# Kernel tuning notes

Measured on AMD Instinct MI355X. Metric: run time of the kernel, lower is better.

## Reference

```python
import jax, jax.numpy as jnp
import numpy as np

N = 50000      # num nodes
E = 500000     # num edges
D = 128        # in_dim == out_dim
H = 8          # num heads
DPH = D // H   # 16, out_dim_per_head
DFF = 2 * D    # FFN hidden
EPS_BN = 1e-5


def setup_inputs() -> dict:
    key = jax.random.key(0)
    ks = jax.random.split(key, 16)
    s = 0.05
    inp = {
        "x": jax.random.normal(ks[0], (N, D), dtype=jnp.float32),
        "edge_index": jax.random.randint(ks[1], (2, E), 0, N, dtype=jnp.int64),
        # attention projections (no bias, use_bias=False); stored as [in, out]
        "WQ": jax.random.normal(ks[2], (D, D), dtype=jnp.float32) * s,
        "WK": jax.random.normal(ks[3], (D, D), dtype=jnp.float32) * s,
        "WV": jax.random.normal(ks[4], (D, D), dtype=jnp.float32) * s,
        # output projection O (has bias by default)
        "WO": jax.random.normal(ks[5], (D, D), dtype=jnp.float32) * s,
        "bO": jnp.zeros((D,), dtype=jnp.float32),
        # FFN
        "W1": jax.random.normal(ks[6], (D, DFF), dtype=jnp.float32) * s,
        "b1": jnp.zeros((DFF,), dtype=jnp.float32),
        "W2": jax.random.normal(ks[7], (DFF, D), dtype=jnp.float32) * s,
        "b2": jnp.zeros((D,), dtype=jnp.float32),
        # batch norms (affine)
        "g1": jnp.ones((D,), dtype=jnp.float32),
        "be1": jnp.zeros((D,), dtype=jnp.float32),
        "g2": jnp.ones((D,), dtype=jnp.float32),
        "be2": jnp.zeros((D,), dtype=jnp.float32),
    }
    return inp


def _batch_norm(h, g, b):
    # training-mode BatchNorm1d over node (batch) dim, biased variance
    mu = jnp.mean(h, axis=0)
    var = jnp.var(h, axis=0)
    return g * (h - mu) * jax.lax.rsqrt(var + EPS_BN) + b


def _forward(x, edge_index, WQ, WK, WV, WO, bO, W1, b1, W2, b2, g1, be1, g2, be2):
    src = edge_index[0]  # j (source / neighbor)
    dst = edge_index[1]  # i (target, softmax segment index)

    Q = (x @ WQ).reshape(N, H, DPH)
    K = (x @ WK).reshape(N, H, DPH)
    V = (x @ WV).reshape(N, H, DPH)

    # edge-wise scores: [E, H]
    score = jnp.sum(Q[dst] * K[src], axis=-1) / jnp.sqrt(jnp.float32(DPH))
    score = jnp.clip(score, -5.0, 5.0)

    # segment softmax over edges grouped by destination node (per head)
    seg_max = jax.ops.segment_max(score, dst, num_segments=N)      # [N, H]
    seg_max = jnp.where(jnp.isfinite(seg_max), seg_max, 0.0)       # empty segs
    ex = jnp.exp(score - seg_max[dst])                             # [E, H]
    seg_sum = jax.ops.segment_sum(ex, dst, num_segments=N)         # [N, H]
    alpha = ex / (seg_sum[dst] + 1e-16)                            # [E, H]

    # weighted message + scatter-add aggregation
    msg = V[src] * alpha[..., None]                                # [E, H, DPH]
    agg = jax.ops.segment_sum(msg, dst, num_segments=N)            # [N, H, DPH]
    h = agg.reshape(N, D)

    # output projection + residual (in_dim == out_dim, no proj) + BN
    h = h @ WO + bO
    h = x + h
    h = _batch_norm(h, g1, be1)

    # FFN + residual + BN
    h2 = h
    h = jax.nn.relu(h @ W1 + b1)
    h = h @ W2 + b2
    h = h2 + h
    h = _batch_norm(h, g2, be2)
    return h


def reference(x, edge_index, WQ, WK, WV, WO, bO, W1, b1, W2, b2, g1, be1, g2, be2):
    return _forward(x, edge_index, WQ, WK, WV, WO, bO, W1, b1, W2, b2, g1, be1, g2, be2)
```

## Files before the change

### kernel.cpp

```cpp
#include <hip/hip_runtime.h>

#define DEV __device__ __forceinline__

constexpr int N = 50000;
constexpr int E = 500000;
constexpr int D = 128;
constexpr int DFF = 256;
constexpr int NBANK = 64;

typedef __attribute__((ext_vector_type(8))) short bfrag8;
typedef __attribute__((ext_vector_type(4))) float f32x4;

DEV unsigned short f2b(float f) {
    unsigned u = __float_as_uint(f);
    unsigned r = (u + 0x7FFFu + ((u >> 16) & 1u)) >> 16;
    return (unsigned short)r;
}
DEV unsigned pack2(float a, float b) {
    return (unsigned)f2b(a) | ((unsigned)f2b(b) << 16);
}
DEV float b2f(unsigned short v) { return __uint_as_float(((unsigned)v) << 16); }
DEV float lo16(unsigned u) { return __uint_as_float(u << 16); }
DEV float hi16(unsigned u) { return __uint_as_float(u & 0xFFFF0000u); }

constexpr float QSCALE = 0.36067376022224085f;
constexpr float CLIP2 = 7.2134752044448170f;

constexpr size_t AL(size_t x) { return (x + 511) & ~(size_t)511; }
constexpr size_t OFF_COUNTS = 0;
constexpr size_t OFF_CURSORS = AL(OFF_COUNTS + (size_t)N * 4);
constexpr size_t OFF_BANK1 = AL(OFF_CURSORS + (size_t)N * 4);
constexpr size_t OFF_BANK2 = AL(OFF_BANK1 + NBANK * 256 * 4);
constexpr size_t OFF_DONE = OFF_BANK2 + NBANK * 256 * 4;
constexpr size_t ZERO_END = OFF_DONE + 512;
constexpr size_t ZW = ZERO_END / 4;
constexpr size_t OFF_OFFS = AL(ZERO_END);
constexpr size_t OFF_BSUM = AL(OFF_OFFS + (size_t)N * 4);
constexpr size_t OFF_BPREF = AL(OFF_BSUM + 1024);
constexpr size_t OFF_SS1 = AL(OFF_BPREF + 1024);
constexpr size_t OFF_SS2 = AL(OFF_SS1 + 1024);
constexpr size_t OFF_B1P = AL(OFF_SS2 + 1024);
constexpr size_t OFF_CSR = AL(OFF_B1P + 1024);
constexpr size_t OFF_WQKVP = AL(OFF_CSR + (size_t)E * 4);
constexpr size_t OFF_WOP = AL(OFF_WQKVP + 49152 * 2);
constexpr size_t OFF_W1PF = AL(OFF_WOP + 16384 * 2);
constexpr size_t OFF_W1P = AL(OFF_W1PF + 32768 * 4);
constexpr size_t OFF_W2P = AL(OFF_W1P + 32768 * 2);
constexpr size_t OFF_Q = AL(OFF_W2P + 32768 * 2);
constexpr size_t OFF_KV = AL(OFF_Q + (size_t)N * 128 * 2);
constexpr size_t OFF_AGG = AL(OFF_KV + (size_t)N * 256 * 2);
constexpr size_t OFF_Y = AL(OFF_AGG + (size_t)N * 128 * 2);
constexpr size_t OFF_T = AL(OFF_Y + (size_t)N * 128 * 2);
constexpr size_t OFF_XB = AL(OFF_T + (size_t)N * 128 * 2);

__global__ void prep_w(const float* __restrict__ WQ, const float* __restrict__ WK,
                       const float* __restrict__ WV, const float* __restrict__ WO,
                       const float* __restrict__ W1, const float* __restrict__ W2,
                       unsigned short* __restrict__ WQKVp, unsigned short* __restrict__ WOp,
                       float* __restrict__ W1pf, unsigned short* __restrict__ W2p,
                       unsigned* __restrict__ zbase) {
    if (blockIdx.x >= 512) {
        size_t i = (size_t)(blockIdx.x - 512) * 256 + threadIdx.x;
        if (i < ZW) zbase[i] = 0u;
        return;
    }
    int gid = blockIdx.x * 256 + threadIdx.x;
    if (gid < 49152) {
        int s = gid >> 14, r = gid & 16383;
        int nt = r >> 11, kb = (r >> 9) & 3, lane = (r >> 3) & 63, j = r & 7;
        int n = nt * 16 + (lane & 15);
        int k = kb * 32 + (lane >> 4) * 8 + j;
        const float* W = (s == 0) ? WQ : (s == 1) ? WK : WV;
        WQKVp[gid] = f2b(W[k * 128 + n]);
    } else if (gid < 65536) {
        int r = gid - 49152;
        int nt = r >> 11, kb = (r >> 9) & 3, lane = (r >> 3) & 63, j = r & 7;
        int n = nt * 16 + (lane & 15);
        int k = kb * 32 + (lane >> 4) * 8 + j;
        WOp[r] = f2b(WO[k * 128 + n]);
    } else if (gid < 98304) {
        int r = gid - 65536;
        int nt = r >> 11, kb = (r >> 9) & 3, lane = (r >> 3) & 63, j = r & 7;
        int n = nt * 16 + (lane & 15);
        int k = kb * 32 + (lane >> 4) * 8 + j;
        W1pf[r] = W1[k * 256 + n];
    } else {
        int r = gid - 98304;
        int nt = r >> 12, kb = (r >> 9) & 7, lane = (r >> 3) & 63, j = r & 7;
        int n = nt * 16 + (lane & 15);
        int k = kb * 32 + (lane >> 4) * 8 + j;
        W2p[r] = f2b(W2[k * 128 + n]);
    }
}

__global__ void scan_a(const int* __restrict__ counts, int* __restrict__ offs,
                       int* __restrict__ bsum, int* __restrict__ bpref,
                       int* __restrict__ done) {
    __shared__ int sm[256];
    __shared__ int ticket;
    int t = threadIdx.x;
    int gi = blockIdx.x * 256 + t;
    int v = (gi < N) ? counts[gi] : 0;
    sm[t] = v;
    __syncthreads();
    for (int o = 1; o < 256; o <<= 1) {
        int x = (t >= o) ? sm[t - o] : 0;
        __syncthreads();
        sm[t] += x;
        __syncthreads();
    }
    if (gi < N) offs[gi] = sm[t] - v;
    if (t == 255) bsum[blockIdx.x] = sm[255];
    __threadfence();
    if (t == 0) ticket = atomicAdd(done, 1);
    __syncthreads();
    if (ticket == (int)gridDim.x - 1) {
        int bv = (t < (int)gridDim.x) ? atomicAdd(&bsum[t], 0) : 0;
        sm[t] = bv;
        __syncthreads();
        for (int o = 1; o < 256; o <<= 1) {
            int x = (t >= o) ? sm[t - o] : 0;
            __syncthreads();
            sm[t] += x;
            __syncthreads();
        }
        bpref[t] = sm[t] - bv;
    }
}

__global__ void fill_k(const int* __restrict__ eidx, const int* __restrict__ offs,
                       const int* __restrict__ bpref,
                       int* __restrict__ cursors, int* __restrict__ csr) {
    int e = blockIdx.x * 256 + threadIdx.x;
    if (e < E) {
        int d = eidx[E + e];
        int p = atomicAdd(&cursors[d], 1);
        csr[offs[d] + bpref[d >> 8] + p] = eidx[e];
    }
}

__global__ __launch_bounds__(256) void qkv_k(const float* __restrict__ x,
                                             const unsigned short* __restrict__ WQKVp,
                                             unsigned short* __restrict__ q,
                                             unsigned short* __restrict__ kv,
                                             unsigned short* __restrict__ xb,
                                             const int* __restrict__ eidx,
                                             int* __restrict__ counts, int nqkv) {
    if ((int)blockIdx.x >= nqkv) {
        int e = ((int)blockIdx.x - nqkv) * 256 + threadIdx.x;
        if (e < E) atomicAdd(&counts[eidx[E + e]], 1);
        return;
    }
    __shared__ unsigned short As[64][136];
    __shared__ unsigned short Cs[64][136];
    const int tid = threadIdx.x;
    const int lane = tid & 63, wave = tid >> 6;
    const int quad = lane >> 4, l15 = lane & 15;
    const int wr = wave >> 1, wc = wave & 1;
    const int row0 = blockIdx.x * 64;

#pragma unroll
    for (int it = 0; it < 4; it++) {
        int c = tid + it * 256;
        int r = c >> 4, k8 = (c & 15) * 8;
        int grow = row0 + r;
        uint4 val = {0u, 0u, 0u, 0u};
        if (grow < N) {
            const float* ap = x + (size_t)grow * 128 + k8;
            float4 f0 = *(const float4*)ap;
            float4 f1 = *(const float4*)(ap + 4);
            val.x = pack2(f0.x, f0.y);
            val.y = pack2(f0.z, f0.w);
            val.z = pack2(f1.x, f1.y);
            val.w = pack2(f1.z, f1.w);
        }
        *(uint4*)&As[r][k8] = val;
    }
    __syncthreads();

#pragma unroll
    for (int j = 0; j < 4; j++) {
        int idx = tid + j * 256;
        int u = idx >> 4, col8 = (idx & 15) * 8;
        int grow = row0 + u;
        if (grow < N) *(uint4*)(xb + (size_t)grow * 128 + col8) = *(const uint4*)&As[u][col8];
    }

    for (int s = 0; s < 3; s++) {
        f32x4 acc[2][4];
#pragma unroll
        for (int i = 0; i < 2; i++)
#pragma unroll
            for (int j = 0; j < 4; j++) acc[i][j] = (f32x4){0.f, 0.f, 0.f, 0.f};
#pragma unroll
        for (int ks = 0; ks < 4; ks++) {
            int k0 = ks * 32 + quad * 8;
            bfrag8 a0 = *(const bfrag8*)&As[wr * 32 + l15][k0];
            bfrag8 a1 = *(const bfrag8*)&As[wr * 32 + 16 + l15][k0];
#pragma unroll
            for (int jn = 0; jn < 4; jn++) {
                int nt = wc * 4 + jn;
                bfrag8 b = *(const bfrag8*)(WQKVp + ((((size_t)s * 8 + nt) * 4 + ks) * 64 + lane) * 8);
                acc[0][jn] = __builtin_amdgcn_mfma_f32_16x16x32_bf16(a0, b, acc[0][jn], 0, 0, 0);
                acc[1][jn] = __builtin_amdgcn_mfma_f32_16x16x32_bf16(a1, b, acc[1][jn], 0, 0, 0);
            }
        }
        if (s) __syncthreads();
        float sc = (s == 0) ? QSCALE : 1.0f;
#pragma unroll
        for (int i = 0; i < 2; i++) {
            int rb = wr * 32 + i * 16 + quad * 4;
#pragma unroll
            for (int jn = 0; jn < 4; jn++) {
                int cl = wc * 64 + jn * 16 + l15;
#pragma unroll
                for (int r = 0; r < 4; r++) Cs[rb + r][cl] = f2b(acc[i][jn][r] * sc);
            }
        }
        __syncthreads();
#pragma unroll
        for (int j = 0; j < 4; j++) {
            int idx = tid + j * 256;
            int u = idx >> 4, col8 = (idx & 15) * 8;
            int grow = row0 + u;
            if (grow < N) {
                uint4 v = *(const uint4*)&Cs[u][col8];
                if (s == 0)
                    *(uint4*)(q + (size_t)grow * 128 + col8) = v;
                else
                    *(uint4*)(kv + (size_t)grow * 256 + (s == 2 ? 128 : 0) + col8) = v;
            }
        }
    }
}

__global__ __launch_bounds__(256) void attn_k(const unsigned short* __restrict__ qb,
                                              const unsigned short* __restrict__ kv,
                                              const int* __restrict__ csr,
                                              const int* __restrict__ offs,
                                              const int* __restrict__ bpref,
                                              const int* __restrict__ counts,
                                              unsigned short* __restrict__ agg) {
    const int wave = threadIdx.x >> 6;
    const int i = blockIdx.x * 4 + wave;
    if (i >= N) return;
    const int lane = threadIdx.x & 63;
    const int slot = lane >> 4;
    const int m = lane & 15;

    uint4 qv = *(const uint4*)(qb + (size_t)i * 128 + m * 8);
    const float q0 = lo16(qv.x), q1 = hi16(qv.x);
    const float q2 = lo16(qv.y), q3 = hi16(qv.y);
    const float q4 = lo16(qv.z), q5 = hi16(qv.z);
    const float q6 = lo16(qv.w), q7 = hi16(qv.w);

    int off = offs[i] + bpref[i >> 8];
    int deg = counts[i];
    const unsigned short* kvm = kv + m * 8;
    float s = 0.f;
    float a0 = 0.f, a1 = 0.f, a2 = 0.f, a3 = 0.f, a4 = 0.f, a5 = 0.f, a6 = 0.f, a7 = 0.f;

    for (int base = 0; base < deg; base += 64) {
        int rem = deg - base;
        if (rem > 64) rem = 64;
        int myj = (lane < rem) ? csr[off + base + lane] : 0;
        for (int e = 0; e < rem; e += 8) {
            int sA = e + slot;
            int jA = __shfl(myj, sA, 64);
            const unsigned short* pA = kvm + (size_t)jA * 256;
            uint4 kA = *(const uint4*)pA;
            uint4 vA = *(const uint4*)(pA + 128);
            bool two = (e + 4) < rem;
            float pdA = (q0 * lo16(kA.x) + q1 * hi16(kA.x)) + (q2 * lo16(kA.y) + q3 * hi16(kA.y)) +
                        (q4 * lo16(kA.z) + q5 * hi16(kA.z)) + (q6 * lo16(kA.w) + q7 * hi16(kA.w));
            pdA += __shfl_xor(pdA, 1, 64);
            float wA = exp2f(fminf(fmaxf(pdA, -CLIP2), CLIP2));
            wA = (sA < rem) ? wA : 0.f;
            if (two) {
                int sB = e + 4 + slot;
                int jB = __shfl(myj, sB, 64);
                const unsigned short* pB = kvm + (size_t)jB * 256;
                uint4 kB = *(const uint4*)pB;
                uint4 vB = *(const uint4*)(pB + 128);
                float pdB = (q0 * lo16(kB.x) + q1 * hi16(kB.x)) + (q2 * lo16(kB.y) + q3 * hi16(kB.y)) +
                            (q4 * lo16(kB.z) + q5 * hi16(kB.z)) + (q6 * lo16(kB.w) + q7 * hi16(kB.w));
                pdB += __shfl_xor(pdB, 1, 64);
                float wB = exp2f(fminf(fmaxf(pdB, -CLIP2), CLIP2));
                wB = (sB < rem) ? wB : 0.f;
                s += wA + wB;
                a0 += wA * lo16(vA.x) + wB * lo16(vB.x);
                a1 += wA * hi16(vA.x) + wB * hi16(vB.x);
                a2 += wA * lo16(vA.y) + wB * lo16(vB.y);
                a3 += wA * hi16(vA.y) + wB * hi16(vB.y);
                a4 += wA * lo16(vA.z) + wB * lo16(vB.z);
                a5 += wA * hi16(vA.z) + wB * hi16(vB.z);
                a6 += wA * lo16(vA.w) + wB * lo16(vB.w);
                a7 += wA * hi16(vA.w) + wB * hi16(vB.w);
            } else {
                s += wA;
                a0 += wA * lo16(vA.x);
                a1 += wA * hi16(vA.x);
                a2 += wA * lo16(vA.y);
                a3 += wA * hi16(vA.y);
                a4 += wA * lo16(vA.z);
                a5 += wA * hi16(vA.z);
                a6 += wA * lo16(vA.w);
                a7 += wA * hi16(vA.w);
            }
        }
    }
#define SLOTRED(v)                 \
    v += __shfl_xor(v, 16, 64);    \
    v += __shfl_xor(v, 32, 64);
    SLOTRED(s)
    SLOTRED(a0) SLOTRED(a1) SLOTRED(a2) SLOTRED(a3)
    SLOTRED(a4) SLOTRED(a5) SLOTRED(a6) SLOTRED(a7)
#undef SLOTRED
    float inv = 1.0f / (s + 1e-16f);
    if (slot == 0) {
        uint4 o;
        o.x = pack2(a0 * inv, a1 * inv);
        o.y = pack2(a2 * inv, a3 * inv);
        o.z = pack2(a4 * inv, a5 * inv);
        o.w = pack2(a6 * inv, a7 * inv);
        *(uint4*)(agg + (size_t)i * 128 + m * 8) = o;
    }
}

__global__ __launch_bounds__(256) void wo_k(const unsigned short* __restrict__ agg,
                                            const unsigned short* __restrict__ WOp,
                                            const unsigned short* __restrict__ xb,
                                            const float* __restrict__ bO,
                                            unsigned short* __restrict__ Yb,
                                            float* __restrict__ bank1) {
    __shared__ unsigned short As[64][136];
    __shared__ unsigned short Xb[64][136];
    __shared__ float Cf[256];
    const int tid = threadIdx.x;
    const int lane = tid & 63, wave = tid >> 6;
    const int quad = lane >> 4, l15 = lane & 15;
    const int wr = wave >> 1, wc = wave & 1;
    const int row0 = blockIdx.x * 64;

    Cf[tid] = 0.f;
#pragma unroll
    for (int it = 0; it < 4; it++) {
        int c = tid + it * 256;
        int r = c >> 4, k8 = (c & 15) * 8;
        int grow = row0 + r;
        uint4 val = {0u, 0u, 0u, 0u};
        uint4 xv = {0u, 0u, 0u, 0u};
        if (grow < N) {
            val = *(const uint4*)(agg + (size_t)grow * 128 + k8);
            xv = *(const uint4*)(xb + (size_t)grow * 128 + k8);
        }
        *(uint4*)&As[r][k8] = val;
        *(uint4*)&Xb[r][k8] = xv;
    }
    __syncthreads();

    f32x4 acc[2][4];
#pragma unroll
    for (int i = 0; i < 2; i++)
#pragma unroll
        for (int j = 0; j < 4; j++) acc[i][j] = (f32x4){0.f, 0.f, 0.f, 0.f};
#pragma unroll
    for (int ks = 0; ks < 4; ks++) {
        int k0 = ks * 32 + quad * 8;
        bfrag8 a0 = *(const bfrag8*)&As[wr * 32 + l15][k0];
        bfrag8 a1 = *(const bfrag8*)&As[wr * 32 + 16 + l15][k0];
#pragma unroll
        for (int jn = 0; jn < 4; jn++) {
            int nt = wc * 4 + jn;
            bfrag8 b = *(const bfrag8*)(WOp + (((size_t)nt * 4 + ks) * 64 + lane) * 8);
            acc[0][jn] = __builtin_amdgcn_mfma_f32_16x16x32_bf16(a0, b, acc[0][jn], 0, 0, 0);
            acc[1][jn] = __builtin_amdgcn_mfma_f32_16x16x32_bf16(a1, b, acc[1][jn], 0, 0, 0);
        }
    }
    __syncthreads();

    unsigned short(*Cs)[136] = As;
    float colS[4] = {0.f, 0.f, 0.f, 0.f}, colQ[4] = {0.f, 0.f, 0.f, 0.f};
#pragma unroll
    for (int i = 0; i < 2; i++) {
        int rb = wr * 32 + i * 16 + quad * 4;
#pragma unroll
        for (int jn = 0; jn < 4; jn++) {
            int cl = wc * 64 + jn * 16 + l15;
            float bv = bO[cl];
#pragma unroll
            for (int r = 0; r < 4; r++) {
                int rl = rb + r;
                float v = acc[i][jn][r] + bv + b2f(Xb[rl][cl]);
                Cs[rl][cl] = f2b(v);
                if (row0 + rl < N) {
                    colS[jn] += v;
                    colQ[jn] += v * v;
                }
            }
        }
    }
#pragma unroll
    for (int jn = 0; jn < 4; jn++) {
        float s = colS[jn], q = colQ[jn];
        s += __shfl_xor(s, 16, 64);
        q += __shfl_xor(q, 16, 64);
        s += __shfl_xor(s, 32, 64);
        q += __shfl_xor(q, 32, 64);
        if (quad == 0) {
            int cl = wc * 64 + jn * 16 + l15;
            atomicAdd(&Cf[cl], s);
            atomicAdd(&Cf[128 + cl], q);
        }
    }
    __syncthreads();
    atomicAdd(&bank1[(size_t)(blockIdx.x & (NBANK - 1)) * 256 + tid], Cf[tid]);
#pragma unroll
    for (int j = 0; j < 4; j++) {
        int idx = tid + j * 256;
        int u = idx >> 4, col8 = (idx & 15) * 8;
        int grow = row0 + u;
        if (grow < N) *(uint4*)(Yb + (size_t)grow * 128 + col8) = *(const uint4*)&Cs[u][col8];
    }
}

__global__ __launch_bounds__(256) void bnscale_k(const float* __restrict__ bank1,
                                                 const float* __restrict__ g, const float* __restrict__ be,
                                                 const float* __restrict__ W1, const float* __restrict__ b1,
                                                 const float* __restrict__ W1pf,
                                                 float* __restrict__ ss, float* __restrict__ b1p,
                                                 unsigned short* __restrict__ W1p) {
    __shared__ float sm[256];
    __shared__ float scl[128];
    __shared__ float shf[128];
    int t = threadIdx.x;
    float s = 0.f;
    for (int cp = 0; cp < NBANK; cp++) s += bank1[cp * 256 + t];
    sm[t] = s;
    __syncthreads();
    if (t < 128) {
        float mu = sm[t] * (1.f / N);
        float var = sm[128 + t] * (1.f / N) - mu * mu;
        float sc = g[t] * rsqrtf(var + 1e-5f);
        float sh = be[t] - mu * sc;
        scl[t] = sc;
        shf[t] = sh;
        if (blockIdx.x == 0) {
            ss[t] = sc;
            ss[128 + t] = sh;
        }
    }
    __syncthreads();
    int i = blockIdx.x * 256 + t;
    int k = ((i >> 9) & 3) * 32 + (((i >> 3) & 63) >> 4) * 8 + (i & 7);
    W1p[i] = f2b(W1pf[i] * scl[k]);
    if (blockIdx.x == 0) {
        float acc = b1[t];
#pragma unroll 4
        for (int kk = 0; kk < 128; kk++) acc += shf[kk] * W1[kk * 256 + t];
        b1p[t] = acc;
    }
}

__global__ __launch_bounds__(256) void ffn_k(const unsigned short* __restrict__ Yb,
                                             const unsigned short* __restrict__ W1p,
                                             const unsigned short* __restrict__ W2p,
                                             const float* __restrict__ ss1,
                                             const float* __restrict__ b1p,
                                             const float* __restrict__ b2,
                                             unsigned short* __restrict__ Tb,
                                             float* __restrict__ bank2) {
    __shared__ unsigned short As[64][136];
    __shared__ unsigned short Zs[64][264];
    __shared__ float Cf[640];
    const int tid = threadIdx.x;
    const int lane = tid & 63, wave = tid >> 6;
    const int quad = lane >> 4, l15 = lane & 15;
    const int wr = wave >> 1, wc = wave & 1;
    const int row0 = blockIdx.x * 64;

    Cf[tid] = ss1[tid];
    Cf[256 + tid] = b1p[tid];
    if (tid < 128) Cf[512 + tid] = b2[tid];
#pragma unroll
    for (int it = 0; it < 4; it++) {
        int c = tid + it * 256;
        int r = c >> 4, k8 = (c & 15) * 8;
        int grow = row0 + r;
        uint4 val = {0u, 0u, 0u, 0u};
        if (grow < N) val = *(const uint4*)(Yb + (size_t)grow * 128 + k8);
        *(uint4*)&As[r][k8] = val;
    }
    __syncthreads();

#pragma unroll
    for (int h = 0; h < 2; h++) {
        f32x4 acc[2][4];
#pragma unroll
        for (int i = 0; i < 2; i++)
#pragma unroll
            for (int j = 0; j < 4; j++) acc[i][j] = (f32x4){0.f, 0.f, 0.f, 0.f};
#pragma unroll
        for (int ks = 0; ks < 4; ks++) {
            int k0 = ks * 32 + quad * 8;
            bfrag8 a0 = *(const bfrag8*)&As[wr * 32 + l15][k0];
            bfrag8 a1 = *(const bfrag8*)&As[wr * 32 + 16 + l15][k0];
#pragma unroll
            for (int jn = 0; jn < 4; jn++) {
                int nt = h * 8 + wc * 4 + jn;
                bfrag8 b = *(const bfrag8*)(W1p + (((size_t)nt * 4 + ks) * 64 + lane) * 8);
                acc[0][jn] = __builtin_amdgcn_mfma_f32_16x16x32_bf16(a0, b, acc[0][jn], 0, 0, 0);
                acc[1][jn] = __builtin_amdgcn_mfma_f32_16x16x32_bf16(a1, b, acc[1][jn], 0, 0, 0);
            }
        }
#pragma unroll
        for (int i = 0; i < 2; i++) {
            int rb = wr * 32 + i * 16 + quad * 4;
#pragma unroll
            for (int jn = 0; jn < 4; jn++) {
                int gc = h * 128 + wc * 64 + jn * 16 + l15;
                float bv = Cf[256 + gc];
#pragma unroll
                for (int r = 0; r < 4; r++)
                    Zs[rb + r][gc] = f2b(fmaxf(acc[i][jn][r] + bv, 0.f));
            }
        }
    }
    __syncthreads();

    f32x4 acc2[2][4];
#pragma unroll
    for (int i = 0; i < 2; i++)
#pragma unroll
        for (int j = 0; j < 4; j++) acc2[i][j] = (f32x4){0.f, 0.f, 0.f, 0.f};
#pragma unroll
    for (int ks = 0; ks < 8; ks++) {
        int k0 = ks * 32 + quad * 8;
        bfrag8 a0 = *(const bfrag8*)&Zs[wr * 32 + l15][k0];
        bfrag8 a1 = *(const bfrag8*)&Zs[wr * 32 + 16 + l15][k0];
#pragma unroll
        for (int jn = 0; jn < 4; jn++) {
            int nt = wc * 4 + jn;
            bfrag8 b = *(const bfrag8*)(W2p + (((size_t)nt * 8 + ks) * 64 + lane) * 8);
            acc2[0][jn] = __builtin_amdgcn_mfma_f32_16x16x32_bf16(a0, b, acc2[0][jn], 0, 0, 0);
            acc2[1][jn] = __builtin_amdgcn_mfma_f32_16x16x32_bf16(a1, b, acc2[1][jn], 0, 0, 0);
        }
    }
    __syncthreads();

    unsigned short(*Ts)[136] = (unsigned short(*)[136]) & Zs[0][0];
    float colS[4] = {0.f, 0.f, 0.f, 0.f}, colQ[4] = {0.f, 0.f, 0.f, 0.f};
#pragma unroll
    for (int i = 0; i < 2; i++) {
        int rb = wr * 32 + i * 16 + quad * 4;
#pragma unroll
        for (int jn = 0; jn < 4; jn++) {
            int cl = wc * 64 + jn * 16 + l15;
            float s1v = Cf[cl], sh1v = Cf[128 + cl], b2v = Cf[512 + cl];
#pragma unroll
            for (int r = 0; r < 4; r++) {
                int rl = rb + r;
                float yv = b2f(As[rl][cl]);
                float v = acc2[i][jn][r] + b2v + yv * s1v + sh1v;
                Ts[rl][cl] = f2b(v);
                if (row0 + rl < N) {
                    colS[jn] += v;
                    colQ[jn] += v * v;
                }
            }
        }
    }
    __syncthreads();
    Cf[tid] = 0.f;
    __syncthreads();
#pragma unroll
    for (int jn = 0; jn < 4; jn++) {
        float s = colS[jn], q = colQ[jn];
        s += __shfl_xor(s, 16, 64);
        q += __shfl_xor(q, 16, 64);
        s += __shfl_xor(s, 32, 64);
        q += __shfl_xor(q, 32, 64);
        if (quad == 0) {
            int cl = wc * 64 + jn * 16 + l15;
            atomicAdd(&Cf[cl], s);
            atomicAdd(&Cf[128 + cl], q);
        }
    }
    __syncthreads();
    atomicAdd(&bank2[(size_t)(blockIdx.x & (NBANK - 1)) * 256 + tid], Cf[tid]);
#pragma unroll
    for (int j = 0; j < 4; j++) {
        int idx = tid + j * 256;
        int u = idx >> 4, col8 = (idx & 15) * 8;
        int grow = row0 + u;
        if (grow < N) *(uint4*)(Tb + (size_t)grow * 128 + col8) = *(const uint4*)&Ts[u][col8];
    }
}

__global__ void bnfin2_k(const float* __restrict__ bank2,
                         const float* __restrict__ g, const float* __restrict__ be,
                         float* __restrict__ ss) {
    __shared__ float sm[256];
    int t = threadIdx.x;
    float s = 0.f;
    for (int cp = 0; cp < NBANK; cp++) s += bank2[cp * 256 + t];
    sm[t] = s;
    __syncthreads();
    if (t < 128) {
        float mu = sm[t] * (1.f / N);
        float var = sm[128 + t] * (1.f / N) - mu * mu;
        float sc = g[t] * rsqrtf(var + 1e-5f);
        ss[t] = sc;
        ss[128 + t] = be[t] - mu * sc;
    }
}

__global__ void bnout_k(const unsigned short* __restrict__ T, const float* __restrict__ ss,
                        float* __restrict__ Out) {
    size_t idx = ((size_t)blockIdx.x * 256 + threadIdx.x) * 8;
    if (idx >= (size_t)N * 128) return;
    int c0 = (int)(idx & 127);
    uint4 tv = *(const uint4*)(T + idx);
    float f[8];
    f[0] = __uint_as_float(tv.x << 16);
    f[1] = __uint_as_float(tv.x & 0xFFFF0000u);
    f[2] = __uint_as_float(tv.y << 16);
    f[3] = __uint_as_float(tv.y & 0xFFFF0000u);
    f[4] = __uint_as_float(tv.z << 16);
    f[5] = __uint_as_float(tv.z & 0xFFFF0000u);
    f[6] = __uint_as_float(tv.w << 16);
    f[7] = __uint_as_float(tv.w & 0xFFFF0000u);
    float4 o0, o1;
    o0.x = f[0] * ss[c0 + 0] + ss[128 + c0 + 0];
    o0.y = f[1] * ss[c0 + 1] + ss[128 + c0 + 1];
    o0.z = f[2] * ss[c0 + 2] + ss[128 + c0 + 2];
    o0.w = f[3] * ss[c0 + 3] + ss[128 + c0 + 3];
    o1.x = f[4] * ss[c0 + 4] + ss[128 + c0 + 4];
    o1.y = f[5] * ss[c0 + 5] + ss[128 + c0 + 5];
    o1.z = f[6] * ss[c0 + 6] + ss[128 + c0 + 6];
    o1.w = f[7] * ss[c0 + 7] + ss[128 + c0 + 7];
    *(float4*)(Out + idx) = o0;
    *(float4*)(Out + idx + 4) = o1;
}

extern "C" void kernel_launch(void* const* d_in, const int* in_sizes, int n_in,
                              void* d_out, int out_size, void* d_ws, size_t ws_size,
                              hipStream_t stream) {
    const float* x = (const float*)d_in[0];
    const int* eidx = (const int*)d_in[1];
    const float* WQ = (const float*)d_in[2];
    const float* WK = (const float*)d_in[3];
    const float* WV = (const float*)d_in[4];
    const float* WO = (const float*)d_in[5];
    const float* bO = (const float*)d_in[6];
    const float* W1 = (const float*)d_in[7];
    const float* b1 = (const float*)d_in[8];
    const float* W2 = (const float*)d_in[9];
    const float* b2 = (const float*)d_in[10];
    const float* g1 = (const float*)d_in[11];
    const float* be1 = (const float*)d_in[12];
    const float* g2 = (const float*)d_in[13];
    const float* be2 = (const float*)d_in[14];
    float* out = (float*)d_out;

    char* ws = (char*)d_ws;
    int* counts = (int*)(ws + OFF_COUNTS);
    int* cursors = (int*)(ws + OFF_CURSORS);
    float* bank1 = (float*)(ws + OFF_BANK1);
    float* bank2 = (float*)(ws + OFF_BANK2);
    int* done = (int*)(ws + OFF_DONE);
    int* offs = (int*)(ws + OFF_OFFS);
    int* bsum = (int*)(ws + OFF_BSUM);
    int* bpref = (int*)(ws + OFF_BPREF);
    float* ss1 = (float*)(ws + OFF_SS1);
    float* ss2 = (float*)(ws + OFF_SS2);
    float* b1p = (float*)(ws + OFF_B1P);
    int* csr = (int*)(ws + OFF_CSR);
    unsigned short* WQKVp = (unsigned short*)(ws + OFF_WQKVP);
    unsigned short* WOp = (unsigned short*)(ws + OFF_WOP);
    float* W1pf = (float*)(ws + OFF_W1PF);
    unsigned short* W1p = (unsigned short*)(ws + OFF_W1P);
    unsigned short* W2p = (unsigned short*)(ws + OFF_W2P);
    unsigned short* qb = (unsigned short*)(ws + OFF_Q);
    unsigned short* kv = (unsigned short*)(ws + OFF_KV);
    unsigned short* agg = (unsigned short*)(ws + OFF_AGG);
    unsigned short* Yb = (unsigned short*)(ws + OFF_Y);
    unsigned short* Tb = (unsigned short*)(ws + OFF_T);
    unsigned short* xb = (unsigned short*)(ws + OFF_XB);

    const int ZB = (int)((ZW + 255) / 256);
    prep_w<<<512 + ZB, 256, 0, stream>>>(WQ, WK, WV, WO, W1, W2, WQKVp, WOp, W1pf, W2p,
                                         (unsigned*)ws);

    const int EB = (E + 255) / 256;
    const int MB64 = (N + 63) / 64;
    qkv_k<<<MB64 + EB, 256, 0, stream>>>(x, WQKVp, qb, kv, xb, eidx, counts, MB64);
    scan_a<<<196, 256, 0, stream>>>(counts, offs, bsum, bpref, done);
    fill_k<<<EB, 256, 0, stream>>>(eidx, offs, bpref, cursors, csr);
    attn_k<<<(N + 3) / 4, 256, 0, stream>>>(qb, kv, csr, offs, bpref, counts, agg);
    wo_k<<<MB64, 256, 0, stream>>>(agg, WOp, xb, bO, Yb, bank1);
    bnscale_k<<<128, 256, 0, stream>>>(bank1, g1, be1, W1, b1, W1pf, ss1, b1p, W1p);
    ffn_k<<<MB64, 256, 0, stream>>>(Yb, W1p, W2p, ss1, b1p, b2, Tb, bank2);
    bnfin2_k<<<1, 256, 0, stream>>>(bank2, g2, be2, ss2);
    bnout_k<<<(int)(((size_t)N * 128 / 8 + 255) / 256), 256, 0, stream>>>(Tb, ss2, out);
}
```

Baseline: 266.1 us.

## Fuse WO projection, BN1, FFN, BN2 into one persistent kernel with grid barriers

Replaces the five tail kernels (wo_k, bnscale_k, ffn_k, bnfin2_k, bnout_k) with a single tail_k that keeps each 64-row tile in LDS and registers across both batch norms, using software grid barriers to wait for the global column statistics. This removes the round trips through Y and T buffers in global memory and several launch gaps. BN1 is now applied to activations directly rather than folded into W1, and the bank count drops to 16. The grid barrier requires all 782 blocks to be co-resident (launch_bounds 256,4); if they are not, the kernel deadlocks.

```diff
diff --git a/kernel.cpp b/kernel.cpp
--- a/kernel.cpp
+++ b/kernel.cpp
@@ -6,7 +6,7 @@
 constexpr int E = 500000;
 constexpr int D = 128;
 constexpr int DFF = 256;
-constexpr int NBANK = 64;
+constexpr int NBANK = 16;
 
 typedef __attribute__((ext_vector_type(8))) short bfrag8;
 typedef __attribute__((ext_vector_type(4))) float f32x4;
@@ -31,33 +31,27 @@
 constexpr size_t OFF_CURSORS = AL(OFF_COUNTS + (size_t)N * 4);
 constexpr size_t OFF_BANK1 = AL(OFF_CURSORS + (size_t)N * 4);
 constexpr size_t OFF_BANK2 = AL(OFF_BANK1 + NBANK * 256 * 4);
-constexpr size_t OFF_DONE = OFF_BANK2 + NBANK * 256 * 4;
+constexpr size_t OFF_DONE = AL(OFF_BANK2 + NBANK * 256 * 4);
 constexpr size_t ZERO_END = OFF_DONE + 512;
 constexpr size_t ZW = ZERO_END / 4;
 constexpr size_t OFF_OFFS = AL(ZERO_END);
 constexpr size_t OFF_BSUM = AL(OFF_OFFS + (size_t)N * 4);
 constexpr size_t OFF_BPREF = AL(OFF_BSUM + 1024);
-constexpr size_t OFF_SS1 = AL(OFF_BPREF + 1024);
-constexpr size_t OFF_SS2 = AL(OFF_SS1 + 1024);
-constexpr size_t OFF_B1P = AL(OFF_SS2 + 1024);
-constexpr size_t OFF_CSR = AL(OFF_B1P + 1024);
+constexpr size_t OFF_CSR = AL(OFF_BPREF + 1024);
 constexpr size_t OFF_WQKVP = AL(OFF_CSR + (size_t)E * 4);
 constexpr size_t OFF_WOP = AL(OFF_WQKVP + 49152 * 2);
-constexpr size_t OFF_W1PF = AL(OFF_WOP + 16384 * 2);
-constexpr size_t OFF_W1P = AL(OFF_W1PF + 32768 * 4);
+constexpr size_t OFF_W1P = AL(OFF_WOP + 16384 * 2);
 constexpr size_t OFF_W2P = AL(OFF_W1P + 32768 * 2);
 constexpr size_t OFF_Q = AL(OFF_W2P + 32768 * 2);
 constexpr size_t OFF_KV = AL(OFF_Q + (size_t)N * 128 * 2);
 constexpr size_t OFF_AGG = AL(OFF_KV + (size_t)N * 256 * 2);
-constexpr size_t OFF_Y = AL(OFF_AGG + (size_t)N * 128 * 2);
-constexpr size_t OFF_T = AL(OFF_Y + (size_t)N * 128 * 2);
-constexpr size_t OFF_XB = AL(OFF_T + (size_t)N * 128 * 2);
+constexpr size_t OFF_XB = AL(OFF_AGG + (size_t)N * 128 * 2);
 
 __global__ void prep_w(const float* __restrict__ WQ, const float* __restrict__ WK,
                        const float* __restrict__ WV, const float* __restrict__ WO,
                        const float* __restrict__ W1, const float* __restrict__ W2,
                        unsigned short* __restrict__ WQKVp, unsigned short* __restrict__ WOp,
-                       float* __restrict__ W1pf, unsigned short* __restrict__ W2p,
+                       unsigned short* __restrict__ W1p, unsigned short* __restrict__ W2p,
                        unsigned* __restrict__ zbase) {
     if (blockIdx.x >= 512) {
         size_t i = (size_t)(blockIdx.x - 512) * 256 + threadIdx.x;
@@ -83,7 +77,7 @@
         int nt = r >> 11, kb = (r >> 9) & 3, lane = (r >> 3) & 63, j = r & 7;
         int n = nt * 16 + (lane & 15);
         int k = kb * 32 + (lane >> 4) * 8 + j;
-        W1pf[r] = W1[k * 256 + n];
+        W1p[r] = f2b(W1[k * 256 + n]);
     } else {
         int r = gid - 98304;
         int nt = r >> 12, kb = (r >> 9) & 7, lane = (r >> 3) & 63, j = r & 7;
@@ -327,174 +321,55 @@
     }
 }
 
-__global__ __launch_bounds__(256) void wo_k(const unsigned short* __restrict__ agg,
-                                            const unsigned short* __restrict__ WOp,
-                                            const unsigned short* __restrict__ xb,
-                                            const float* __restrict__ bO,
-                                            unsigned short* __restrict__ Yb,
-                                            float* __restrict__ bank1) {
+DEV void gbarrier(int* gb, int nb) {
+    __syncthreads();
+    __threadfence();
+    if (threadIdx.x == 0) {
+        __hip_atomic_fetch_add(gb, 1, __ATOMIC_RELEASE, __HIP_MEMORY_SCOPE_AGENT);
+        while (__hip_atomic_load(gb, __ATOMIC_RELAXED, __HIP_MEMORY_SCOPE_AGENT) < nb)
+            __builtin_amdgcn_s_sleep(8);
+    }
+    __syncthreads();
+    __threadfence();
+}
+
+__global__ __launch_bounds__(256, 4) void tail_k(
+    const unsigned short* __restrict__ agg, const unsigned short* __restrict__ WOp,
+    const unsigned short* __restrict__ xb, const float* __restrict__ bO,
+    const float* __restrict__ b1, const float* __restrict__ b2,
+    const unsigned short* __restrict__ W1p, const unsigned short* __restrict__ W2p,
+    const float* __restrict__ g1, const float* __restrict__ be1,
+    const float* __restrict__ g2, const float* __restrict__ be2,
+    float* __restrict__ bank1, float* __restrict__ bank2,
+    int* __restrict__ gbar, float* __restrict__ out) {
     __shared__ unsigned short As[64][136];
-    __shared__ unsigned short Xb[64][136];
-    __shared__ float Cf[256];
-    const int tid = threadIdx.x;
-    const int lane = tid & 63, wave = tid >> 6;
-    const int quad = lane >> 4, l15 = lane & 15;
-    const int wr = wave >> 1, wc = wave & 1;
-    const int row0 = blockIdx.x * 64;
-
-    Cf[tid] = 0.f;
-#pragma unroll
-    for (int it = 0; it < 4; it++) {
-        int c = tid + it * 256;
-        int r = c >> 4, k8 = (c & 15) * 8;
-        int grow = row0 + r;
-        uint4 val = {0u, 0u, 0u, 0u};
-        uint4 xv = {0u, 0u, 0u, 0u};
-        if (grow < N) {
-            val = *(const uint4*)(agg + (size_t)grow * 128 + k8);
-            xv = *(const uint4*)(xb + (size_t)grow * 128 + k8);
-        }
-        *(uint4*)&As[r][k8] = val;
-        *(uint4*)&Xb[r][k8] = xv;
-    }
-    __syncthreads();
-
-    f32x4 acc[2][4];
-#pragma unroll
-    for (int i = 0; i < 2; i++)
-#pragma unroll
-        for (int j = 0; j < 4; j++) acc[i][j] = (f32x4){0.f, 0.f, 0.f, 0.f};
-#pragma unroll
-    for (int ks = 0; ks < 4; ks++) {
-        int k0 = ks * 32 + quad * 8;
-        bfrag8 a0 = *(const bfrag8*)&As[wr * 32 + l15][k0];
-        bfrag8 a1 = *(const bfrag8*)&As[wr * 32 + 16 + l15][k0];
-#pragma unroll
-        for (int jn = 0; jn < 4; jn++) {
-            int nt = wc * 4 + jn;
-            bfrag8 b = *(const bfrag8*)(WOp + (((size_t)nt * 4 + ks) * 64 + lane) * 8);
-            acc[0][jn] = __builtin_amdgcn_mfma_f32_16x16x32_bf16(a0, b, acc[0][jn], 0, 0, 0);
-            acc[1][jn] = __builtin_amdgcn_mfma_f32_16x16x32_bf16(a1, b, acc[1][jn], 0, 0, 0);
-        }
-    }
-    __syncthreads();
-
-    unsigned short(*Cs)[136] = As;
-    float colS[4] = {0.f, 0.f, 0.f, 0.f}, colQ[4] = {0.f, 0.f, 0.f, 0.f};
-#pragma unroll
-    for (int i = 0; i < 2; i++) {
-        int rb = wr * 32 + i * 16 + quad * 4;
-#pragma unroll
-        for (int jn = 0; jn < 4; jn++) {
-            int cl = wc * 64 + jn * 16 + l15;
-            float bv = bO[cl];
-#pragma unroll
-            for (int r = 0; r < 4; r++) {
-                int rl = rb + r;
-                float v = acc[i][jn][r] + bv + b2f(Xb[rl][cl]);
-                Cs[rl][cl] = f2b(v);
-                if (row0 + rl < N) {
-                    colS[jn] += v;
-                    colQ[jn] += v * v;
-                }
-            }
-        }
-    }
-#pragma unroll
-    for (int jn = 0; jn < 4; jn++) {
-        float s = colS[jn], q = colQ[jn];
-        s += __shfl_xor(s, 16, 64);
-        q += __shfl_xor(q, 16, 64);
-        s += __shfl_xor(s, 32, 64);
-        q += __shfl_xor(q, 32, 64);
-        if (quad == 0) {
-            int cl = wc * 64 + jn * 16 + l15;
-            atomicAdd(&Cf[cl], s);
-            atomicAdd(&Cf[128 + cl], q);
-        }
-    }
-    __syncthreads();
-    atomicAdd(&bank1[(size_t)(blockIdx.x & (NBANK - 1)) * 256 + tid], Cf[tid]);
-#pragma unroll
-    for (int j = 0; j < 4; j++) {
-        int idx = tid + j * 256;
-        int u = idx >> 4, col8 = (idx & 15) * 8;
-        int grow = row0 + u;
-        if (grow < N) *(uint4*)(Yb + (size_t)grow * 128 + col8) = *(const uint4*)&Cs[u][col8];
-    }
-}
-
-__global__ __launch_bounds__(256) void bnscale_k(const float* __restrict__ bank1,
-                                                 const float* __restrict__ g, const float* __restrict__ be,
-                                                 const float* __restrict__ W1, const float* __restrict__ b1,
-                                                 const float* __restrict__ W1pf,
-                                                 float* __restrict__ ss, float* __restrict__ b1p,
-                                                 unsigned short* __restrict__ W1p) {
-    __shared__ float sm[256];
-    __shared__ float scl[128];
-    __shared__ float shf[128];
-    int t = threadIdx.x;
-    float s = 0.f;
-    for (int cp = 0; cp < NBANK; cp++) s += bank1[cp * 256 + t];
-    sm[t] = s;
-    __syncthreads();
-    if (t < 128) {
-        float mu = sm[t] * (1.f / N);
-        float var = sm[128 + t] * (1.f / N) - mu * mu;
-        float sc = g[t] * rsqrtf(var + 1e-5f);
-        float sh = be[t] - mu * sc;
-        scl[t] = sc;
-        shf[t] = sh;
-        if (blockIdx.x == 0) {
-            ss[t] = sc;
-            ss[128 + t] = sh;
-        }
-    }
-    __syncthreads();
-    int i = blockIdx.x * 256 + t;
-    int k = ((i >> 9) & 3) * 32 + (((i >> 3) & 63) >> 4) * 8 + (i & 7);
-    W1p[i] = f2b(W1pf[i] * scl[k]);
-    if (blockIdx.x == 0) {
-        float acc = b1[t];
-#pragma unroll 4
-        for (int kk = 0; kk < 128; kk++) acc += shf[kk] * W1[kk * 256 + t];
-        b1p[t] = acc;
-    }
-}
-
-__global__ __launch_bounds__(256) void ffn_k(const unsigned short* __restrict__ Yb,
-                                             const unsigned short* __restrict__ W1p,
-                                             const unsigned short* __restrict__ W2p,
-                                             const float* __restrict__ ss1,
-                                             const float* __restrict__ b1p,
-                                             const float* __restrict__ b2,
-                                             unsigned short* __restrict__ Tb,
-                                             float* __restrict__ bank2) {
-    __shared__ unsigned short As[64][136];
-    __shared__ unsigned short Zs[64][264];
+    __shared__ unsigned short Xs[64][136];
     __shared__ float Cf[640];
     const int tid = threadIdx.x;
     const int lane = tid & 63, wave = tid >> 6;
     const int quad = lane >> 4, l15 = lane & 15;
     const int wr = wave >> 1, wc = wave & 1;
     const int row0 = blockIdx.x * 64;
-
-    Cf[tid] = ss1[tid];
-    Cf[256 + tid] = b1p[tid];
-    if (tid < 128) Cf[512 + tid] = b2[tid];
+    const int NB = (int)gridDim.x;
+
+    Cf[tid] = 0.f;
 #pragma unroll
     for (int it = 0; it < 4; it++) {
         int c = tid + it * 256;
         int r = c >> 4, k8 = (c & 15) * 8;
         int grow = row0 + r;
-        uint4 val = {0u, 0u, 0u, 0u};
-        if (grow < N) val = *(const uint4*)(Yb + (size_t)grow * 128 + k8);
-        *(uint4*)&As[r][k8] = val;
-    }
-    __syncthreads();
-
-#pragma unroll
-    for (int h = 0; h < 2; h++) {
+        uint4 av = {0u, 0u, 0u, 0u};
+        uint4 xv = {0u, 0u, 0u, 0u};
+        if (grow < N) {
+            av = *(const uint4*)(agg + (size_t)grow * 128 + k8);
+            xv = *(const uint4*)(xb + (size_t)grow * 128 + k8);
+        }
+        *(uint4*)&As[r][k8] = av;
+        *(uint4*)&Xs[r][k8] = xv;
+    }
+    __syncthreads();
+
+    {
         f32x4 acc[2][4];
 #pragma unroll
         for (int i = 0; i < 2; i++)
@@ -507,140 +382,214 @@
             bfrag8 a1 = *(const bfrag8*)&As[wr * 32 + 16 + l15][k0];
 #pragma unroll
             for (int jn = 0; jn < 4; jn++) {
-                int nt = h * 8 + wc * 4 + jn;
-                bfrag8 b = *(const bfrag8*)(W1p + (((size_t)nt * 4 + ks) * 64 + lane) * 8);
+                int nt = wc * 4 + jn;
+                bfrag8 b = *(const bfrag8*)(WOp + (((size_t)nt * 4 + ks) * 64 + lane) * 8);
                 acc[0][jn] = __builtin_amdgcn_mfma_f32_16x16x32_bf16(a0, b, acc[0][jn], 0, 0, 0);
                 acc[1][jn] = __builtin_amdgcn_mfma_f32_16x16x32_bf16(a1, b, acc[1][jn], 0, 0, 0);
             }
         }
+        __syncthreads();
+
+        float colS[4] = {0.f, 0.f, 0.f, 0.f}, colQ[4] = {0.f, 0.f, 0.f, 0.f};
 #pragma unroll
         for (int i = 0; i < 2; i++) {
             int rb = wr * 32 + i * 16 + quad * 4;
 #pragma unroll
             for (int jn = 0; jn < 4; jn++) {
-                int gc = h * 128 + wc * 64 + jn * 16 + l15;
-                float bv = Cf[256 + gc];
-#pragma unroll
-                for (int r = 0; r < 4; r++)
-                    Zs[rb + r][gc] = f2b(fmaxf(acc[i][jn][r] + bv, 0.f));
-            }
-        }
-    }
-    __syncthreads();
-
-    f32x4 acc2[2][4];
-#pragma unroll
-    for (int i = 0; i < 2; i++)
-#pragma unroll
-        for (int j = 0; j < 4; j++) acc2[i][j] = (f32x4){0.f, 0.f, 0.f, 0.f};
-#pragma unroll
-    for (int ks = 0; ks < 8; ks++) {
-        int k0 = ks * 32 + quad * 8;
-        bfrag8 a0 = *(const bfrag8*)&Zs[wr * 32 + l15][k0];
-        bfrag8 a1 = *(const bfrag8*)&Zs[wr * 32 + 16 + l15][k0];
+                int cl = wc * 64 + jn * 16 + l15;
+                float bv = bO[cl];
+#pragma unroll
+                for (int r = 0; r < 4; r++) {
+                    int rl = rb + r;
+                    float v = acc[i][jn][r] + bv + b2f(Xs[rl][cl]);
+                    As[rl][cl] = f2b(v);
+                    if (row0 + rl < N) {
+                        colS[jn] += v;
+                        colQ[jn] += v * v;
+                    }
+                }
+            }
+        }
 #pragma unroll
         for (int jn = 0; jn < 4; jn++) {
-            int nt = wc * 4 + jn;
-            bfrag8 b = *(const bfrag8*)(W2p + (((size_t)nt * 8 + ks) * 64 + lane) * 8);
-            acc2[0][jn] = __builtin_amdgcn_mfma_f32_16x16x32_bf16(a0, b, acc2[0][jn], 0, 0, 0);
-            acc2[1][jn] = __builtin_amdgcn_mfma_f32_16x16x32_bf16(a1, b, acc2[1][jn], 0, 0, 0);
-        }
-    }
-    __syncthreads();
-
-    unsigned short(*Ts)[136] = (unsigned short(*)[136]) & Zs[0][0];
-    float colS[4] = {0.f, 0.f, 0.f, 0.f}, colQ[4] = {0.f, 0.f, 0.f, 0.f};
-#pragma unroll
-    for (int i = 0; i < 2; i++) {
-        int rb = wr * 32 + i * 16 + quad * 4;
-#pragma unroll
-        for (int jn = 0; jn < 4; jn++) {
-            int cl = wc * 64 + jn * 16 + l15;
-            float s1v = Cf[cl], sh1v = Cf[128 + cl], b2v = Cf[512 + cl];
-#pragma unroll
-            for (int r = 0; r < 4; r++) {
-                int rl = rb + r;
-                float yv = b2f(As[rl][cl]);
-                float v = acc2[i][jn][r] + b2v + yv * s1v + sh1v;
-                Ts[rl][cl] = f2b(v);
-                if (row0 + rl < N) {
-                    colS[jn] += v;
-                    colQ[jn] += v * v;
-                }
-            }
-        }
-    }
-    __syncthreads();
-    Cf[tid] = 0.f;
-    __syncthreads();
-#pragma unroll
-    for (int jn = 0; jn < 4; jn++) {
-        float s = colS[jn], q = colQ[jn];
-        s += __shfl_xor(s, 16, 64);
-        q += __shfl_xor(q, 16, 64);
-        s += __shfl_xor(s, 32, 64);
-        q += __shfl_xor(q, 32, 64);
-        if (quad == 0) {
-            int cl = wc * 64 + jn * 16 + l15;
-            atomicAdd(&Cf[cl], s);
-            atomicAdd(&Cf[128 + cl], q);
-        }
-    }
-    __syncthreads();
-    atomicAdd(&bank2[(size_t)(blockIdx.x & (NBANK - 1)) * 256 + tid], Cf[tid]);
+            float s = colS[jn], q = colQ[jn];
+            s += __shfl_xor(s, 16, 64);
+            q += __shfl_xor(q, 16, 64);
+            s += __shfl_xor(s, 32, 64);
+            q += __shfl_xor(q, 32, 64);
+            if (quad == 0) {
+                int cl = wc * 64 + jn * 16 + l15;
+                atomicAdd(&Cf[cl], s);
+                atomicAdd(&Cf[128 + cl], q);
+            }
+        }
+        __syncthreads();
+        atomicAdd(&bank1[(size_t)(blockIdx.x & (NBANK - 1)) * 256 + tid], Cf[tid]);
+    }
+
+    gbarrier(&gbar[0], NB);
+
+    {
+        float s = 0.f;
+        for (int cp = 0; cp < NBANK; cp++) s += bank1[cp * 256 + tid];
+        Cf[256 + tid] = s;
+    }
+    __syncthreads();
+    if (tid < 128) {
+        float mu = Cf[256 + tid] * (1.f / N);
+        float var = Cf[384 + tid] * (1.f / N) - mu * mu;
+        float sc = g1[tid] * rsqrtf(var + 1e-5f);
+        Cf[tid] = sc;
+        Cf[128 + tid] = be1[tid] - mu * sc;
+    }
+    __syncthreads();
 #pragma unroll
     for (int j = 0; j < 4; j++) {
         int idx = tid + j * 256;
         int u = idx >> 4, col8 = (idx & 15) * 8;
-        int grow = row0 + u;
-        if (grow < N) *(uint4*)(Tb + (size_t)grow * 128 + col8) = *(const uint4*)&Ts[u][col8];
-    }
-}
-
-__global__ void bnfin2_k(const float* __restrict__ bank2,
-                         const float* __restrict__ g, const float* __restrict__ be,
-                         float* __restrict__ ss) {
-    __shared__ float sm[256];
-    int t = threadIdx.x;
-    float s = 0.f;
-    for (int cp = 0; cp < NBANK; cp++) s += bank2[cp * 256 + t];
-    sm[t] = s;
-    __syncthreads();
-    if (t < 128) {
-        float mu = sm[t] * (1.f / N);
-        float var = sm[128 + t] * (1.f / N) - mu * mu;
-        float sc = g[t] * rsqrtf(var + 1e-5f);
-        ss[t] = sc;
-        ss[128 + t] = be[t] - mu * sc;
-    }
-}
-
-__global__ void bnout_k(const unsigned short* __restrict__ T, const float* __restrict__ ss,
-                        float* __restrict__ Out) {
-    size_t idx = ((size_t)blockIdx.x * 256 + threadIdx.x) * 8;
-    if (idx >= (size_t)N * 128) return;
-    int c0 = (int)(idx & 127);
-    uint4 tv = *(const uint4*)(T + idx);
-    float f[8];
-    f[0] = __uint_as_float(tv.x << 16);
-    f[1] = __uint_as_float(tv.x & 0xFFFF0000u);
-    f[2] = __uint_as_float(tv.y << 16);
-    f[3] = __uint_as_float(tv.y & 0xFFFF0000u);
-    f[4] = __uint_as_float(tv.z << 16);
-    f[5] = __uint_as_float(tv.z & 0xFFFF0000u);
-    f[6] = __uint_as_float(tv.w << 16);
-    f[7] = __uint_as_float(tv.w & 0xFFFF0000u);
-    float4 o0, o1;
-    o0.x = f[0] * ss[c0 + 0] + ss[128 + c0 + 0];
-    o0.y = f[1] * ss[c0 + 1] + ss[128 + c0 + 1];
-    o0.z = f[2] * ss[c0 + 2] + ss[128 + c0 + 2];
-    o0.w = f[3] * ss[c0 + 3] + ss[128 + c0 + 3];
-    o1.x = f[4] * ss[c0 + 4] + ss[128 + c0 + 4];
-    o1.y = f[5] * ss[c0 + 5] + ss[128 + c0 + 5];
-    o1.z = f[6] * ss[c0 + 6] + ss[128 + c0 + 6];
-    o1.w = f[7] * ss[c0 + 7] + ss[128 + c0 + 7];
-    *(float4*)(Out + idx) = o0;
-    *(float4*)(Out + idx + 4) = o1;
+        uint4 v = *(const uint4*)&As[u][col8];
+        uint4 o;
+        o.x = pack2(lo16(v.x) * Cf[col8 + 0] + Cf[128 + col8 + 0],
+                    hi16(v.x) * Cf[col8 + 1] + Cf[128 + col8 + 1]);
+        o.y = pack2(lo16(v.y) * Cf[col8 + 2] + Cf[128 + col8 + 2],
+                    hi16(v.y) * Cf[col8 + 3] + Cf[128 + col8 + 3]);
+        o.z = pack2(lo16(v.z) * Cf[col8 + 4] + Cf[128 + col8 + 4],
+                    hi16(v.z) * Cf[col8 + 5] + Cf[128 + col8 + 5]);
+        o.w = pack2(lo16(v.w) * Cf[col8 + 6] + Cf[128 + col8 + 6],
+                    hi16(v.w) * Cf[col8 + 7] + Cf[128 + col8 + 7]);
+        *(uint4*)&As[u][col8] = o;
+    }
+    __syncthreads();
+    Cf[tid] = 0.f;
+    Cf[256 + tid] = b1[tid];
+    if (tid < 128) Cf[512 + tid] = b2[tid];
+    __syncthreads();
+
+    f32x4 acc2[2][4];
+#pragma unroll
+    for (int i = 0; i < 2; i++)
+#pragma unroll
+        for (int j = 0; j < 4; j++) acc2[i][j] = (f32x4){0.f, 0.f, 0.f, 0.f};
+
+#pragma unroll
+    for (int h = 0; h < 2; h++) {
+        f32x4 a1c[2][4];
+#pragma unroll
+        for (int i = 0; i < 2; i++)
+#pragma unroll
+            for (int j = 0; j < 4; j++) a1c[i][j] = (f32x4){0.f, 0.f, 0.f, 0.f};
+#pragma unroll
+        for (int ks = 0; ks < 4; ks++) {
+            int k0 = ks * 32 + quad * 8;
+            bfrag8 a0 = *(const bfrag8*)&As[wr * 32 + l15][k0];
+            bfrag8 a1 = *(const bfrag8*)&As[wr * 32 + 16 + l15][k0];
+#pragma unroll
+            for (int jn = 0; jn < 4; jn++) {
+                int nt = h * 8 + wc * 4 + jn;
+                bfrag8 b = *(const bfrag8*)(W1p + (((size_t)nt * 4 + ks) * 64 + lane) * 8);
+                a1c[0][jn] = __builtin_amdgcn_mfma_f32_16x16x32_bf16(a0, b, a1c[0][jn], 0, 0, 0);
+                a1c[1][jn] = __builtin_amdgcn_mfma_f32_16x16x32_bf16(a1, b, a1c[1][jn], 0, 0, 0);
+            }
+        }
+#pragma unroll
+        for (int i = 0; i < 2; i++) {
+            int rb = wr * 32 + i * 16 + quad * 4;
+#pragma unroll
+            for (int jn = 0; jn < 4; jn++) {
+                int gc = wc * 64 + jn * 16 + l15;
+                float bv = Cf[256 + h * 128 + gc];
+#pragma unroll
+                for (int r = 0; r < 4; r++)
+                    Xs[rb + r][gc] = f2b(fmaxf(a1c[i][jn][r] + bv, 0.f));
+            }
+        }
+        __syncthreads();
+#pragma unroll
+        for (int ks2 = 0; ks2 < 4; ks2++) {
+            int k0 = ks2 * 32 + quad * 8;
+            int ksg = h * 4 + ks2;
+            bfrag8 a0 = *(const bfrag8*)&Xs[wr * 32 + l15][k0];
+            bfrag8 a1 = *(const bfrag8*)&Xs[wr * 32 + 16 + l15][k0];
+#pragma unroll
+            for (int jn = 0; jn < 4; jn++) {
+                int nt = wc * 4 + jn;
+                bfrag8 b = *(const bfrag8*)(W2p + (((size_t)nt * 8 + ksg) * 64 + lane) * 8);
+                acc2[0][jn] = __builtin_amdgcn_mfma_f32_16x16x32_bf16(a0, b, acc2[0][jn], 0, 0, 0);
+                acc2[1][jn] = __builtin_amdgcn_mfma_f32_16x16x32_bf16(a1, b, acc2[1][jn], 0, 0, 0);
+            }
+        }
+        __syncthreads();
+    }
+
+    {
+        float colS[4] = {0.f, 0.f, 0.f, 0.f}, colQ[4] = {0.f, 0.f, 0.f, 0.f};
+#pragma unroll
+        for (int i = 0; i < 2; i++) {
+            int rb = wr * 32 + i * 16 + quad * 4;
+#pragma unroll
+            for (int jn = 0; jn < 4; jn++) {
+                int cl = wc * 64 + jn * 16 + l15;
+                float b2v = Cf[512 + cl];
+#pragma unroll
+                for (int r = 0; r < 4; r++) {
+                    int rl = rb + r;
+                    float v = acc2[i][jn][r] + b2v + b2f(As[rl][cl]);
+                    acc2[i][jn][r] = v;
+                    if (row0 + rl < N) {
+                        colS[jn] += v;
+                        colQ[jn] += v * v;
+                    }
+                }
+            }
+        }
+#pragma unroll
+        for (int jn = 0; jn < 4; jn++) {
+            float s = colS[jn], q = colQ[jn];
+            s += __shfl_xor(s, 16, 64);
+            q += __shfl_xor(q, 16, 64);
+            s += __shfl_xor(s, 32, 64);
+            q += __shfl_xor(q, 32, 64);
+            if (quad == 0) {
+                int cl = wc * 64 + jn * 16 + l15;
+                atomicAdd(&Cf[cl], s);
+                atomicAdd(&Cf[128 + cl], q);
+            }
+        }
+        __syncthreads();
+        atomicAdd(&bank2[(size_t)(blockIdx.x & (NBANK - 1)) * 256 + tid], Cf[tid]);
+    }
+
+    gbarrier(&gbar[32], NB);
+
+    {
+        float s = 0.f;
+        for (int cp = 0; cp < NBANK; cp++) s += bank2[cp * 256 + tid];
+        Cf[256 + tid] = s;
+    }
+    __syncthreads();
+    if (tid < 128) {
+        float mu = Cf[256 + tid] * (1.f / N);
+        float var = Cf[384 + tid] * (1.f / N) - mu * mu;
+        float sc = g2[tid] * rsqrtf(var + 1e-5f);
+        Cf[tid] = sc;
+        Cf[128 + tid] = be2[tid] - mu * sc;
+    }
+    __syncthreads();
+
+#pragma unroll
+    for (int i = 0; i < 2; i++) {
+        int rb = wr * 32 + i * 16 + quad * 4;
+#pragma unroll
+        for (int jn = 0; jn < 4; jn++) {
+            int cl = wc * 64 + jn * 16 + l15;
+            float sc = Cf[cl], sh = Cf[128 + cl];
+#pragma unroll
+            for (int r = 0; r < 4; r++) {
+                int grow = row0 + rb + r;
+                if (grow < N) out[(size_t)grow * 128 + cl] = acc2[i][jn][r] * sc + sh;
+            }
+        }
+    }
 }
 
 extern "C" void kernel_launch(void* const* d_in, const int* in_sizes, int n_in,
@@ -669,27 +618,22 @@
     float* bank1 = (float*)(ws + OFF_BANK1);
     float* bank2 = (float*)(ws + OFF_BANK2);
     int* done = (int*)(ws + OFF_DONE);
+    int* gbar = (int*)(ws + OFF_DONE + 64);
     int* offs = (int*)(ws + OFF_OFFS);
     int* bsum = (int*)(ws + OFF_BSUM);
     int* bpref = (int*)(ws + OFF_BPREF);
-    float* ss1 = (float*)(ws + OFF_SS1);
-    float* ss2 = (float*)(ws + OFF_SS2);
-    float* b1p = (float*)(ws + OFF_B1P);
     int* csr = (int*)(ws + OFF_CSR);
     unsigned short* WQKVp = (unsigned short*)(ws + OFF_WQKVP);
     unsigned short* WOp = (unsigned short*)(ws + OFF_WOP);
-    float* W1pf = (float*)(ws + OFF_W1PF);
     unsigned short* W1p = (unsigned short*)(ws + OFF_W1P);
     unsigned short* W2p = (unsigned short*)(ws + OFF_W2P);
     unsigned short* qb = (unsigned short*)(ws + OFF_Q);
     unsigned short* kv = (unsigned short*)(ws + OFF_KV);
     unsigned short* agg = (unsigned short*)(ws + OFF_AGG);
-    unsigned short* Yb = (unsigned short*)(ws + OFF_Y);
-    unsigned short* Tb = (unsigned short*)(ws + OFF_T);
     unsigned short* xb = (unsigned short*)(ws + OFF_XB);
 
     const int ZB = (int)((ZW + 255) / 256);
-    prep_w<<<512 + ZB, 256, 0, stream>>>(WQ, WK, WV, WO, W1, W2, WQKVp, WOp, W1pf, W2p,
+    prep_w<<<512 + ZB, 256, 0, stream>>>(WQ, WK, WV, WO, W1, W2, WQKVp, WOp, W1p, W2p,
                                          (unsigned*)ws);
 
     const int EB = (E + 255) / 256;
@@ -698,9 +642,6 @@
     scan_a<<<196, 256, 0, stream>>>(counts, offs, bsum, bpref, done);
     fill_k<<<EB, 256, 0, stream>>>(eidx, offs, bpref, cursors, csr);
     attn_k<<<(N + 3) / 4, 256, 0, stream>>>(qb, kv, csr, offs, bpref, counts, agg);
-    wo_k<<<MB64, 256, 0, stream>>>(agg, WOp, xb, bO, Yb, bank1);
-    bnscale_k<<<128, 256, 0, stream>>>(bank1, g1, be1, W1, b1, W1pf, ss1, b1p, W1p);
-    ffn_k<<<MB64, 256, 0, stream>>>(Yb, W1p, W2p, ss1, b1p, b2, Tb, bank2);
-    bnfin2_k<<<1, 256, 0, stream>>>(bank2, g2, be2, ss2);
-    bnout_k<<<(int)(((size_t)N * 128 / 8 + 255) / 256), 256, 0, stream>>>(Tb, ss2, out);
-}
+    tail_k<<<MB64, 256, 0, stream>>>(agg, WOp, xb, bO, b1, b2, W1p, W2p,
+                                     g1, be1, g2, be2, bank1, bank2, gbar, out);
+}
```

Result: slower. 489.3 us (+83.9%).
